# Kernel optimization log

Measured on AMD Instinct MI355X. Metric: run time of the kernel, lower is better.

The kernel has to match this reference:

```python
import jax, jax.numpy as jnp
import numpy as np

B, C, H, W = 32, 256, 64, 64
EPS = 1e-8  # clamp for cosine-similarity denominators


def setup_inputs() -> dict:
    key = jax.random.key(0)
    k1, k2, k3 = jax.random.split(key, 3)
    unmasked = jax.random.normal(k1, (B, C, H, W), dtype=jnp.float32)
    masked = jax.random.normal(k2, (B, C, H, W), dtype=jnp.float32)
    latent_mask = jax.random.randint(k3, (B, H, W), 0, 2, dtype=jnp.int32)
    return {
        "unmasked_latent_tensors": unmasked,
        "masked_latent_tensors": masked,
        "latent_mask": latent_mask,
    }


def reference(unmasked_latent_tensors, masked_latent_tensors, latent_mask):
    # Original torch code builds a full [B, B*H*W, H, W] cross-activation of a
    # cosine-similarity 1x1 conv (input vs. every masked position used as a
    # prototype), then gathers only the diagonal entries where batch index and
    # spatial position match. Mathematically that diagonal is just the
    # per-position cosine similarity along the channel axis, computed here
    # directly.
    u = unmasked_latent_tensors
    m = masked_latent_tensors
    num = jnp.sum(u * m, axis=1)                       # [B, H, W]
    u_norm = jnp.sqrt(jnp.sum(u * u, axis=1))          # [B, H, W]
    m_norm = jnp.sqrt(jnp.sum(m * m, axis=1))          # [B, H, W]
    sim = num / (jnp.maximum(u_norm, EPS) * jnp.maximum(m_norm, EPS))
    # masked=True: average similarity over mask==1 positions.
    mask_f = (latent_mask != 0).astype(sim.dtype)      # [B, H, W]
    return jnp.sum(sim * mask_f) / jnp.sum(mask_f)
```

## Files before the change

kernel.cpp:

```cpp
#include <hip/hip_runtime.h>


#define BB    32
#define CC    256
#define HH    64
#define WW    64
#define HWSZ  (HH * WW)
#define NPOS  (BB * HWSZ)
#define CSPLIT 8
#define CPER  (CC / CSPLIT)
#define PGPB  32
#define POSPB (PGPB * 4)
#define SIM_EPS 1e-8f

__global__ __launch_bounds__(256, 4) void
sim_reduce_kernel(const float* __restrict__ u,
                  const float* __restrict__ m,
                  const int* __restrict__ mask,
                  double* __restrict__ ws)
{
    __shared__ float lds_num[CSPLIT * POSPB];
    __shared__ float lds_uu [CSPLIT * POSPB];
    __shared__ float lds_mm [CSPLIT * POSPB];

    const int tid    = threadIdx.x;
    const int posgrp = tid & (PGPB - 1);
    const int cchunk = tid >> 5;

    const int p0 = blockIdx.x * POSPB + posgrp * 4;
    const int b  = p0 >> 12;
    const int hw = p0 & (HWSZ - 1);

    const size_t base = (size_t)b * CC * HWSZ + (size_t)cchunk * CPER * HWSZ + hw;
    const float4* up = (const float4*)(u + base);
    const float4* mp = (const float4*)(m + base);

    float4 num = {0.f, 0.f, 0.f, 0.f};
    float4 uu  = {0.f, 0.f, 0.f, 0.f};
    float4 mm  = {0.f, 0.f, 0.f, 0.f};

#pragma unroll 8
    for (int c = 0; c < CPER; ++c) {
        const float4 a = up[(size_t)c * (HWSZ / 4)];
        const float4 v = mp[(size_t)c * (HWSZ / 4)];
        num.x = fmaf(a.x, v.x, num.x); num.y = fmaf(a.y, v.y, num.y);
        num.z = fmaf(a.z, v.z, num.z); num.w = fmaf(a.w, v.w, num.w);
        uu.x  = fmaf(a.x, a.x, uu.x);  uu.y  = fmaf(a.y, a.y, uu.y);
        uu.z  = fmaf(a.z, a.z, uu.z);  uu.w  = fmaf(a.w, a.w, uu.w);
        mm.x  = fmaf(v.x, v.x, mm.x);  mm.y  = fmaf(v.y, v.y, mm.y);
        mm.z  = fmaf(v.z, v.z, mm.z);  mm.w  = fmaf(v.w, v.w, mm.w);
    }

    ((float4*)lds_num)[cchunk * PGPB + posgrp] = num;
    ((float4*)lds_uu )[cchunk * PGPB + posgrp] = uu;
    ((float4*)lds_mm )[cchunk * PGPB + posgrp] = mm;
    __syncthreads();

    double sd = 0.0, md = 0.0;
    if (tid < POSPB) {
        float n = 0.f, su = 0.f, sm = 0.f;
#pragma unroll
        for (int cc = 0; cc < CSPLIT; ++cc) {
            n  += lds_num[cc * POSPB + tid];
            su += lds_uu [cc * POSPB + tid];
            sm += lds_mm [cc * POSPB + tid];
        }
        const float denom = fmaxf(sqrtf(su), SIM_EPS) * fmaxf(sqrtf(sm), SIM_EPS);
        const float sim   = n / denom;
        const int   mk    = (mask[blockIdx.x * POSPB + tid] != 0) ? 1 : 0;
        sd = mk ? (double)sim : 0.0;
        md = (double)mk;
    }

#pragma unroll
    for (int off = 32; off > 0; off >>= 1) {
        sd += __shfl_down(sd, off, 64);
        md += __shfl_down(md, off, 64);
    }

    __shared__ double red_s[4];
    __shared__ double red_m[4];
    const int wave = tid >> 6;
    const int lane = tid & 63;
    if (lane == 0) { red_s[wave] = sd; red_m[wave] = md; }
    __syncthreads();

    if (tid == 0) {
        const double ts = red_s[0] + red_s[1] + red_s[2] + red_s[3];
        const double tm = red_m[0] + red_m[1] + red_m[2] + red_m[3];
        atomicAdd(&ws[0], ts);
        atomicAdd(&ws[1], tm);
    }
}

__global__ void finalize_kernel(const double* __restrict__ ws,
                                float* __restrict__ out)
{
    out[0] = (float)(ws[0] / ws[1]);
}

extern "C" void kernel_launch(void* const* d_in, const int* in_sizes, int n_in,
                              void* d_out, int out_size, void* d_ws, size_t ws_size,
                              hipStream_t stream)
{
    const float* u    = (const float*)d_in[0];
    const float* m    = (const float*)d_in[1];
    const int*   mask = (const int*)d_in[2];
    float*  out = (float*)d_out;
    double* ws  = (double*)d_ws;

    hipMemsetAsync(d_ws, 0, 2 * sizeof(double), stream);

    sim_reduce_kernel<<<NPOS / POSPB, 256, 0, stream>>>(u, m, mask, ws);
    finalize_kernel<<<1, 1, 0, stream>>>(ws, out);
}
```

Measured before the change: 284.1 us.

## Split channels 16 ways and issue all loads up front before accumulating

Each block now covers 64 positions with the channel axis split 16 ways instead of 128 positions split 8 ways. Each thread loads all 16 of its u and m float4 values into registers before doing any FMAs, so more memory requests are in flight per thread. The end-of-block reduction drops to a single wave doing a shuffle reduction and the atomics, which removes the second LDS stage and one barrier. The trade-offs are twice as many blocks, so twice as many double-precision atomics, and higher register use now that the occupancy hint in launch bounds is gone.

```diff
diff --git a/kernel.cpp b/kernel.cpp
--- a/kernel.cpp
+++ b/kernel.cpp
@@ -7,13 +7,13 @@
 #define WW    64
 #define HWSZ  (HH * WW)
 #define NPOS  (BB * HWSZ)
-#define CSPLIT 8
+#define CSPLIT 16
 #define CPER  (CC / CSPLIT)
-#define PGPB  32
+#define PGPB  16
 #define POSPB (PGPB * 4)
 #define SIM_EPS 1e-8f
 
-__global__ __launch_bounds__(256, 4) void
+__global__ __launch_bounds__(256) void
 sim_reduce_kernel(const float* __restrict__ u,
                   const float* __restrict__ m,
                   const int* __restrict__ mask,
@@ -25,7 +25,7 @@
 
     const int tid    = threadIdx.x;
     const int posgrp = tid & (PGPB - 1);
-    const int cchunk = tid >> 5;
+    const int cchunk = tid >> 4;
 
     const int p0 = blockIdx.x * POSPB + posgrp * 4;
     const int b  = p0 >> 12;
@@ -35,20 +35,23 @@
     const float4* up = (const float4*)(u + base);
     const float4* mp = (const float4*)(m + base);
 
+    float4 a[CPER], v[CPER];
+#pragma unroll
+    for (int c = 0; c < CPER; ++c) a[c] = up[(size_t)c * (HWSZ / 4)];
+#pragma unroll
+    for (int c = 0; c < CPER; ++c) v[c] = mp[(size_t)c * (HWSZ / 4)];
+
     float4 num = {0.f, 0.f, 0.f, 0.f};
     float4 uu  = {0.f, 0.f, 0.f, 0.f};
     float4 mm  = {0.f, 0.f, 0.f, 0.f};
-
-#pragma unroll 8
+#pragma unroll
     for (int c = 0; c < CPER; ++c) {
-        const float4 a = up[(size_t)c * (HWSZ / 4)];
-        const float4 v = mp[(size_t)c * (HWSZ / 4)];
-        num.x = fmaf(a.x, v.x, num.x); num.y = fmaf(a.y, v.y, num.y);
-        num.z = fmaf(a.z, v.z, num.z); num.w = fmaf(a.w, v.w, num.w);
-        uu.x  = fmaf(a.x, a.x, uu.x);  uu.y  = fmaf(a.y, a.y, uu.y);
-        uu.z  = fmaf(a.z, a.z, uu.z);  uu.w  = fmaf(a.w, a.w, uu.w);
-        mm.x  = fmaf(v.x, v.x, mm.x);  mm.y  = fmaf(v.y, v.y, mm.y);
-        mm.z  = fmaf(v.z, v.z, mm.z);  mm.w  = fmaf(v.w, v.w, mm.w);
+        num.x = fmaf(a[c].x, v[c].x, num.x); num.y = fmaf(a[c].y, v[c].y, num.y);
+        num.z = fmaf(a[c].z, v[c].z, num.z); num.w = fmaf(a[c].w, v[c].w, num.w);
+        uu.x  = fmaf(a[c].x, a[c].x, uu.x);  uu.y  = fmaf(a[c].y, a[c].y, uu.y);
+        uu.z  = fmaf(a[c].z, a[c].z, uu.z);  uu.w  = fmaf(a[c].w, a[c].w, uu.w);
+        mm.x  = fmaf(v[c].x, v[c].x, mm.x);  mm.y  = fmaf(v[c].y, v[c].y, mm.y);
+        mm.z  = fmaf(v[c].z, v[c].z, mm.z);  mm.w  = fmaf(v[c].w, v[c].w, mm.w);
     }
 
     ((float4*)lds_num)[cchunk * PGPB + posgrp] = num;
@@ -56,7 +59,6 @@
     ((float4*)lds_mm )[cchunk * PGPB + posgrp] = mm;
     __syncthreads();
 
-    double sd = 0.0, md = 0.0;
     if (tid < POSPB) {
         float n = 0.f, su = 0.f, sm = 0.f;
 #pragma unroll
@@ -68,28 +70,17 @@
         const float denom = fmaxf(sqrtf(su), SIM_EPS) * fmaxf(sqrtf(sm), SIM_EPS);
         const float sim   = n / denom;
         const int   mk    = (mask[blockIdx.x * POSPB + tid] != 0) ? 1 : 0;
-        sd = mk ? (double)sim : 0.0;
-        md = (double)mk;
-    }
-
+        double sd = mk ? (double)sim : 0.0;
+        double md = (double)mk;
 #pragma unroll
-    for (int off = 32; off > 0; off >>= 1) {
-        sd += __shfl_down(sd, off, 64);
-        md += __shfl_down(md, off, 64);
-    }
-
-    __shared__ double red_s[4];
-    __shared__ double red_m[4];
-    const int wave = tid >> 6;
-    const int lane = tid & 63;
-    if (lane == 0) { red_s[wave] = sd; red_m[wave] = md; }
-    __syncthreads();
-
-    if (tid == 0) {
-        const double ts = red_s[0] + red_s[1] + red_s[2] + red_s[3];
-        const double tm = red_m[0] + red_m[1] + red_m[2] + red_m[3];
-        atomicAdd(&ws[0], ts);
-        atomicAdd(&ws[1], tm);
+        for (int off = 32; off > 0; off >>= 1) {
+            sd += __shfl_down(sd, off, 64);
+            md += __shfl_down(md, off, 64);
+        }
+        if (tid == 0) {
+            atomicAdd(&ws[0], sd);
+            atomicAdd(&ws[1], md);
+        }
     }
 }
 
```

New measurement: 282.9 us. Within noise of the previous version (-0.4%).
